# Kernel optimization log

Measured on AMD Instinct MI355X. Metric: run time of the kernel, lower is better.

## Reference

```python
import jax, jax.numpy as jnp
import numpy as np

HID = 4096
BLOCK = 64


def _masks(n=HID, bs=BLOCK):
    blk = jnp.arange(n) // bs
    mask_diag = (blk[:, None] == blk[None, :]).astype(jnp.float32)  # block-diagonal ones
    triu = (jnp.arange(n)[:, None] <= jnp.arange(n)[None, :]).astype(jnp.float32)
    mask_triu = triu * (1.0 - mask_diag)  # strictly above-block upper triangle
    return mask_diag, mask_triu


def _mc_linear(x, W, b, mask_diag, mask_triu):
    # A uses detached input (stop_gradient); B carries gradient through x.
    A = jax.lax.stop_gradient(x) @ (W * mask_triu)
    B = x @ (W * mask_diag)
    return A + B + b


def setup_inputs() -> dict:
    key = jax.random.key(0)
    ks = jax.random.split(key, 10)
    X = jax.random.normal(ks[0], (8192, 1024), dtype=jnp.float32)
    s_in = 1.0 / np.sqrt(1024)
    s_h = 1.0 / np.sqrt(HID)
    W0 = jax.random.normal(ks[1], (1024, HID), dtype=jnp.float32) * s_in
    b0 = jax.random.normal(ks[2], (HID,), dtype=jnp.float32) * s_in
    W1 = jax.random.normal(ks[3], (HID, HID), dtype=jnp.float32) * s_h
    b1 = jax.random.normal(ks[4], (HID,), dtype=jnp.float32) * s_h
    W2 = jax.random.normal(ks[5], (HID, HID), dtype=jnp.float32) * s_h
    b2 = jax.random.normal(ks[6], (HID,), dtype=jnp.float32) * s_h
    W3 = jax.random.normal(ks[7], (HID, HID), dtype=jnp.float32) * s_h
    b3 = jax.random.normal(ks[8], (HID,), dtype=jnp.float32) * s_h
    return {"X": X, "W0": W0, "b0": b0, "W1": W1, "b1": b1,
            "W2": W2, "b2": b2, "W3": W3, "b3": b3}


def reference(X, W0, b0, W1, b1, W2, b2, W3, b3):
    mask_diag, mask_triu = _masks()
    h = X @ W0 + b0  # [B, HID]
    for W, b in ((W1, b1), (W2, b2), (W3, b3)):
        h = jax.nn.relu(h)  # dropout=0.0 -> identity
        h = _mc_linear(h, W, b, mask_diag, mask_triu)
    y_pred = h[..., BLOCK - 1::BLOCK]  # [B, num_blocks]
    return y_pred[..., -1]  # level = -1 (default LEVEL)
```

## Files before the change

### kernel.cpp

```cpp
#include <hip/hip_runtime.h>

typedef unsigned short u16;
typedef __attribute__((ext_vector_type(8))) short short8;
typedef __attribute__((ext_vector_type(4))) float f32x4;
typedef __attribute__((ext_vector_type(4))) unsigned short us4;

__device__ __forceinline__ u16 f2bf(float f) {
    unsigned u = __float_as_uint(f);
    u += 0x7fffu + ((u >> 16) & 1u);
    return (u16)(u >> 16);
}
__device__ __forceinline__ float bf2f(u16 h) {
    return __uint_as_float(((unsigned)h) << 16);
}

__global__ __launch_bounds__(256) void k_cvt(const float* __restrict__ in,
                                             u16* __restrict__ out, long n) {
    long i = ((long)blockIdx.x * 256 + threadIdx.x) * 4;
    if (i >= n) return;
    float4 v = *(const float4*)(in + i);
    us4 o;
    o.x = f2bf(v.x); o.y = f2bf(v.y); o.z = f2bf(v.z); o.w = f2bf(v.w);
    *(us4*)(out + i) = o;
}

__global__ __launch_bounds__(256) void k_transpose(const float* __restrict__ W,
                                                   u16* __restrict__ Wt,
                                                   int K, int N, int mask) {
    __shared__ float tile[32][33];
    const int n0 = blockIdx.x * 32, k0 = blockIdx.y * 32;
    const int tx = threadIdx.x, ty = threadIdx.y;
    if (mask && ((k0 >> 6) > (n0 >> 6))) {
        if (k0 >= ((n0 >> 8) + 1) * 256) return;
#pragma unroll
        for (int j = 0; j < 32; j += 8)
            Wt[(size_t)(n0 + ty + j) * K + (k0 + tx)] = 0;
        return;
    }
#pragma unroll
    for (int j = 0; j < 32; j += 8)
        tile[ty + j][tx] = W[(size_t)(k0 + ty + j) * N + (n0 + tx)];
    __syncthreads();
#pragma unroll
    for (int j = 0; j < 32; j += 8)
        Wt[(size_t)(n0 + ty + j) * K + (k0 + tx)] = f2bf(tile[tx][ty + j]);
}

__global__ __launch_bounds__(256) void k_extract(const float* __restrict__ W3,
                                                 float* __restrict__ col, int N) {
    int k = blockIdx.x * 256 + threadIdx.x;
    col[k] = W3[(size_t)k * N + (N - 1)];
}

#define BM 256
#define BN 256
#define BK 32
#define BUFE 16384
#define GLDS(src, dst)                                                          \
    __builtin_amdgcn_global_load_lds(                                           \
        (const __attribute__((address_space(1))) void*)(src),                   \
        (__attribute__((address_space(3))) void*)(dst), 16, 0, 0)

__global__ __launch_bounds__(512, 2) void k_gemm(const u16* __restrict__ A,
                                                 const u16* __restrict__ Bt,
                                                 const float* __restrict__ bias,
                                                 u16* __restrict__ C,
                                                 int M, int N, int K, int varK) {
    __shared__ __align__(16) u16 lds[4 * BUFE];

    const int d = blockIdx.y * gridDim.x + blockIdx.x;
    int bx, by;
    if (varK) {
        bx = (int)gridDim.x - 1 - (d / (int)gridDim.y);
        by = d % (int)gridDim.y;
    } else {
        const int nwg = (int)(gridDim.x * gridDim.y);
        const int cpx = nwg >> 3;
        const int swz = (d & 7) * cpx + (d >> 3);
        bx = swz % (int)gridDim.x;
        by = swz / (int)gridDim.x;
    }

    const int tid = (int)threadIdx.x;
    const int lane = tid & 63, wv = tid >> 6;
    const int wm = wv >> 2, wn = wv & 3;
    const int keff = varK ? min(K, (bx + 1) * BN) : K;
    const int nt = keff >> 5;

    const u16* Ab = A + (size_t)by * BM * K;
    const u16* Bb = Bt + (size_t)bx * BN * K;

    const int tr = tid >> 2, ts = tid & 3;
    const int ss = ts ^ ((tr >> 1) & 3);
    const u16* aSrc = Ab + (size_t)tr * K + ss * 8;
    const u16* bSrc = Bb + (size_t)tr * K + ss * 8;

#define STA(tt, ci, dbuf) GLDS(aSrc + (size_t)(tt) * BK + (size_t)(ci) * 128 * K, \
                               lds + (dbuf) + (ci) * 4096 + tid * 8)
#define STB(tt, ci, dbuf) GLDS(bSrc + (size_t)(tt) * BK + (size_t)(ci) * 128 * K, \
                               lds + (dbuf) + 8192 + (ci) * 4096 + tid * 8)

    const int l15 = lane & 15;
    const int sw = (lane >> 4) ^ ((l15 >> 1) & 3);
    const int arow = wm * 128 + l15;
    const int brow = wn * 64 + l15;

#define RDA(dst, mfh, dbuf)                                                          \
    {                                                                                \
        _Pragma("unroll")                                                            \
        for (int i = 0; i < 4; ++i)                                                  \
            dst[i] = *(const short8*)(lds + (dbuf) + (arow + (mfh) * 64 + i * 16) * 32 \
                                      + sw * 8);                                     \
    }
#define RDB(dst, dbuf)                                                               \
    {                                                                                \
        _Pragma("unroll")                                                            \
        for (int nf = 0; nf < 4; ++nf)                                               \
            dst[nf] = *(const short8*)(lds + (dbuf) + 8192 + (brow + nf * 16) * 32   \
                                       + sw * 8);                                    \
    }
#define MFMA16(afS, bfS, mb)                                                         \
    {                                                                                \
        __builtin_amdgcn_s_setprio(1);                                              \
        _Pragma("unroll")                                                            \
        for (int i = 0; i < 4; ++i)                                                  \
            _Pragma("unroll")                                                        \
            for (int nf = 0; nf < 4; ++nf)                                           \
                acc[(mb) + i][nf] = __builtin_amdgcn_mfma_f32_16x16x32_bf16(         \
                    afS[i], bfS[nf], acc[(mb) + i][nf], 0, 0, 0);                    \
        __builtin_amdgcn_s_setprio(0);                                              \
    }
#define PHASE_END                                                 \
    __builtin_amdgcn_sched_barrier(0);                            \
    __builtin_amdgcn_s_barrier();                                 \
    __builtin_amdgcn_sched_barrier(0);
#define VMW(n)                                                    \
    __builtin_amdgcn_sched_barrier(0);                            \
    asm volatile("s_waitcnt vmcnt(" #n ")");                      \
    __builtin_amdgcn_sched_barrier(0);

    f32x4 acc[8][4];
#pragma unroll
    for (int i = 0; i < 8; ++i)
#pragma unroll
        for (int j = 0; j < 4; ++j)
            acc[i][j] = (f32x4){0.f, 0.f, 0.f, 0.f};

    short8 afX[4], afY[4], bfP[4], bfQ[4];

    STA(0, 0, 0);     STA(0, 1, 0);     STB(0, 0, 0);     STB(0, 1, 0);
    STA(1, 0, BUFE);  STA(1, 1, BUFE);  STB(1, 0, BUFE);  STB(1, 1, BUFE);
    STA(2, 0, 2*BUFE);STA(2, 1, 2*BUFE);STB(2, 0, 2*BUFE);STB(2, 1, 2*BUFE);
    VMW(8)
    __builtin_amdgcn_s_barrier();
    __builtin_amdgcn_sched_barrier(0);
    RDA(afX, 0, 0);
    RDB(bfP, 0);

    for (int T = 0; T < nt; T += 2) {
        const int U = T + 1;
        const int bT = (T & 3) * BUFE;
        const int bU = ((T + 1) & 3) * BUFE;
        const int bV = ((T + 2) & 3) * BUFE;
        const int bZ1 = ((T + 3) & 3) * BUFE;
        const int bZ2 = ((T + 4) & 3) * BUFE;
        RDA(afY, 1, bT);
        if (T + 3 < nt) { STA(T + 3, 0, bZ1); STA(T + 3, 1, bZ1); }
        MFMA16(afX, bfP, 0);
        if (T + 3 < nt) { VMW(6) } else { VMW(0) }
        PHASE_END;
        RDA(afX, 0, bU);
        RDB(bfQ, bU);
        if (T + 3 < nt) { STB(T + 3, 0, bZ1); STB(T + 3, 1, bZ1); }
        MFMA16(afY, bfP, 4);
        PHASE_END;
        RDA(afY, 1, bU);
        if (U + 3 < nt) { STA(U + 3, 0, bZ2); STA(U + 3, 1, bZ2); }
        MFMA16(afX, bfQ, 0);
        if (U + 1 < nt) {
            if (U + 3 < nt) { VMW(6) } else if (U + 2 < nt) { VMW(4) } else { VMW(0) }
        }
        PHASE_END;
        if (U + 1 < nt) {
            RDA(afX, 0, bV);
            RDB(bfP, bV);
        }
        if (U + 3 < nt) { STB(U + 3, 0, bZ2); STB(U + 3, 1, bZ2); }
        MFMA16(afY, bfQ, 4);
        PHASE_END;
    }

    const int rbase = by * BM + wm * 128 + (lane >> 4) * 4;
    const int cbase = bx * BN + wn * 64 + l15;
#pragma unroll
    for (int nf = 0; nf < 4; ++nf) {
        const int gc = cbase + nf * 16;
        const float bv = bias[gc];
#pragma unroll
        for (int mf = 0; mf < 8; ++mf) {
#pragma unroll
            for (int r = 0; r < 4; ++r) {
                int gr = rbase + mf * 16 + r;
                float h = acc[mf][nf][r] + bv;
                h = fmaxf(h, 0.0f);
                C[(size_t)gr * N + gc] = f2bf(h);
            }
        }
    }
#undef STA
#undef STB
#undef RDA
#undef RDB
#undef MFMA16
#undef PHASE_END
#undef VMW
}

__global__ __launch_bounds__(256) void k_matvec(const u16* __restrict__ act,
                                                const float* __restrict__ col,
                                                const float* __restrict__ b3,
                                                float* __restrict__ out, int K) {
    const int m = blockIdx.x, t = (int)threadIdx.x;
    const u16* row = act + (size_t)m * K;
    float acc = 0.f;
#pragma unroll
    for (int j = 0; j < 2; ++j) {
        int base = t * 16 + j * 8;
        short8 v = *(const short8*)(row + base);
#pragma unroll
        for (int u = 0; u < 8; ++u)
            acc += bf2f((u16)v[u]) * col[base + u];
    }
#pragma unroll
    for (int off = 32; off > 0; off >>= 1)
        acc += __shfl_down(acc, off);
    __shared__ float red[4];
    if ((t & 63) == 0) red[t >> 6] = acc;
    __syncthreads();
    if (t == 0) out[m] = red[0] + red[1] + red[2] + red[3] + b3[K - 1];
}

extern "C" void kernel_launch(void* const* d_in, const int* in_sizes, int n_in,
                              void* d_out, int out_size, void* d_ws, size_t ws_size,
                              hipStream_t stream) {
    const float* X  = (const float*)d_in[0];
    const float* W0 = (const float*)d_in[1];
    const float* b0 = (const float*)d_in[2];
    const float* W1 = (const float*)d_in[3];
    const float* b1 = (const float*)d_in[4];
    const float* W2 = (const float*)d_in[5];
    const float* b2 = (const float*)d_in[6];
    const float* W3 = (const float*)d_in[7];
    const float* b3 = (const float*)d_in[8];
    float* out = (float*)d_out;

    const int M = 8192, K0 = 1024, H = 4096;

    char* ws = (char*)d_ws;
    u16* Wt    = (u16*)(ws);
    u16* actA  = (u16*)(ws + 33554432);
    u16* actB  = (u16*)(ws + 33554432 + 67108864);
    u16* Xb    = actB;
    float* col = (float*)(ws + 33554432 + 2 * 67108864);

    k_cvt<<<dim3((M * K0) / 1024), 256, 0, stream>>>(X, Xb, (long)M * K0);
    k_transpose<<<dim3(H / 32, K0 / 32), dim3(32, 8), 0, stream>>>(W0, Wt, K0, H, 0);
    k_gemm<<<dim3(H / BN, M / BM), 512, 0, stream>>>(Xb, Wt, b0, actA, M, H, K0, 0);
    k_transpose<<<dim3(H / 32, H / 32), dim3(32, 8), 0, stream>>>(W1, Wt, H, H, 1);
    k_gemm<<<dim3(H / BN, M / BM), 512, 0, stream>>>(actA, Wt, b1, actB, M, H, H, 1);
    k_transpose<<<dim3(H / 32, H / 32), dim3(32, 8), 0, stream>>>(W2, Wt, H, H, 1);
    k_gemm<<<dim3(H / BN, M / BM), 512, 0, stream>>>(actB, Wt, b2, actA, M, H, H, 1);
    k_extract<<<dim3(H / 256), 256, 0, stream>>>(W3, col, H);
    k_matvec<<<dim3(M), 256, 0, stream>>>(actA, col, b3, out, H);
}
```

Before: 406.2 us.

## Switch GEMM inner loop from 16x16x32 to 32x32x16 bf16 MFMA

Replaces the per-wave 128x64 tile's 16x16x32 MFMA tiling with 32x32x16 MFMAs (4x2 fragments of f32x16 accumulators), splitting each 32-wide K tile into two K-halves per phase. LDS fragment reads and the swizzle indexing change to match the 32-row operand layout, the main loop drops from two tiles to one tile per iteration, and the epilogue row mapping is rewritten for the 32x32 output layout. The aim is fewer MFMA issues and fewer LDS fragment loads per FLOP, at the cost of a changed barrier cadence and different LDS bank-conflict behaviour.

```diff
diff --git a/kernel.cpp b/kernel.cpp
--- a/kernel.cpp
+++ b/kernel.cpp
@@ -2,7 +2,7 @@
 
 typedef unsigned short u16;
 typedef __attribute__((ext_vector_type(8))) short short8;
-typedef __attribute__((ext_vector_type(4))) float f32x4;
+typedef __attribute__((ext_vector_type(16))) float f32x16;
 typedef __attribute__((ext_vector_type(4))) unsigned short us4;
 
 __device__ __forceinline__ u16 f2bf(float f) {
@@ -100,34 +100,35 @@
 #define STB(tt, ci, dbuf) GLDS(bSrc + (size_t)(tt) * BK + (size_t)(ci) * 128 * K, \
                                lds + (dbuf) + 8192 + (ci) * 4096 + tid * 8)
 
-    const int l15 = lane & 15;
-    const int sw = (lane >> 4) ^ ((l15 >> 1) & 3);
-    const int arow = wm * 128 + l15;
-    const int brow = wn * 64 + l15;
-
-#define RDA(dst, mfh, dbuf)                                                          \
+    const int l31 = lane & 31, l5 = lane >> 5;
+    const int sw2 = (l31 >> 1) & 3;
+    const int sbase = l5 ^ sw2;
+    const int arow = wm * 128 + l31;
+    const int brow = wn * 64 + l31;
+
+#define RDA(dst, ks, dbuf)                                                           \
     {                                                                                \
         _Pragma("unroll")                                                            \
-        for (int i = 0; i < 4; ++i)                                                  \
-            dst[i] = *(const short8*)(lds + (dbuf) + (arow + (mfh) * 64 + i * 16) * 32 \
-                                      + sw * 8);                                     \
-    }
-#define RDB(dst, dbuf)                                                               \
+        for (int mf = 0; mf < 4; ++mf)                                               \
+            dst[mf] = *(const short8*)(lds + (dbuf) + (arow + mf * 32) * 32          \
+                                       + ((sbase ^ ((ks) << 1))) * 8);               \
+    }
+#define RDB(dst, ks, dbuf)                                                           \
     {                                                                                \
         _Pragma("unroll")                                                            \
-        for (int nf = 0; nf < 4; ++nf)                                               \
-            dst[nf] = *(const short8*)(lds + (dbuf) + 8192 + (brow + nf * 16) * 32   \
-                                       + sw * 8);                                    \
-    }
-#define MFMA16(afS, bfS, mb)                                                         \
+        for (int nf = 0; nf < 2; ++nf)                                               \
+            dst[nf] = *(const short8*)(lds + (dbuf) + 8192 + (brow + nf * 32) * 32   \
+                                       + ((sbase ^ ((ks) << 1))) * 8);               \
+    }
+#define MFMA8(afS, bfS)                                                              \
     {                                                                                \
         __builtin_amdgcn_s_setprio(1);                                              \
         _Pragma("unroll")                                                            \
-        for (int i = 0; i < 4; ++i)                                                  \
+        for (int mf = 0; mf < 4; ++mf)                                               \
             _Pragma("unroll")                                                        \
-            for (int nf = 0; nf < 4; ++nf)                                           \
-                acc[(mb) + i][nf] = __builtin_amdgcn_mfma_f32_16x16x32_bf16(         \
-                    afS[i], bfS[nf], acc[(mb) + i][nf], 0, 0, 0);                    \
+            for (int nf = 0; nf < 2; ++nf)                                           \
+                acc[mf][nf] = __builtin_amdgcn_mfma_f32_32x32x16_bf16(               \
+                    afS[mf], bfS[nf], acc[mf][nf], 0, 0, 0);                         \
         __builtin_amdgcn_s_setprio(0);                                              \
     }
 #define PHASE_END                                                 \
@@ -139,14 +140,16 @@
     asm volatile("s_waitcnt vmcnt(" #n ")");                      \
     __builtin_amdgcn_sched_barrier(0);
 
-    f32x4 acc[8][4];
-#pragma unroll
-    for (int i = 0; i < 8; ++i)
-#pragma unroll
-        for (int j = 0; j < 4; ++j)
-            acc[i][j] = (f32x4){0.f, 0.f, 0.f, 0.f};
-
-    short8 afX[4], afY[4], bfP[4], bfQ[4];
+    f32x16 acc[4][2];
+#pragma unroll
+    for (int i = 0; i < 4; ++i)
+#pragma unroll
+        for (int j = 0; j < 2; ++j)
+#pragma unroll
+            for (int r = 0; r < 16; ++r)
+                acc[i][j][r] = 0.f;
+
+    short8 afX[4], afY[4], bfX[2], bfY[2];
 
     STA(0, 0, 0);     STA(0, 1, 0);     STB(0, 0, 0);     STB(0, 1, 0);
     STA(1, 0, BUFE);  STA(1, 1, BUFE);  STB(1, 0, BUFE);  STB(1, 1, BUFE);
@@ -155,53 +158,41 @@
     __builtin_amdgcn_s_barrier();
     __builtin_amdgcn_sched_barrier(0);
     RDA(afX, 0, 0);
-    RDB(bfP, 0);
-
-    for (int T = 0; T < nt; T += 2) {
-        const int U = T + 1;
+    RDB(bfX, 0, 0);
+
+    for (int T = 0; T < nt; ++T) {
         const int bT = (T & 3) * BUFE;
-        const int bU = ((T + 1) & 3) * BUFE;
-        const int bV = ((T + 2) & 3) * BUFE;
-        const int bZ1 = ((T + 3) & 3) * BUFE;
-        const int bZ2 = ((T + 4) & 3) * BUFE;
+        const int bY = ((T + 1) & 3) * BUFE;
+        const int bZ = ((T + 3) & 3) * BUFE;
         RDA(afY, 1, bT);
-        if (T + 3 < nt) { STA(T + 3, 0, bZ1); STA(T + 3, 1, bZ1); }
-        MFMA16(afX, bfP, 0);
-        if (T + 3 < nt) { VMW(6) } else { VMW(0) }
-        PHASE_END;
-        RDA(afX, 0, bU);
-        RDB(bfQ, bU);
-        if (T + 3 < nt) { STB(T + 3, 0, bZ1); STB(T + 3, 1, bZ1); }
-        MFMA16(afY, bfP, 4);
-        PHASE_END;
-        RDA(afY, 1, bU);
-        if (U + 3 < nt) { STA(U + 3, 0, bZ2); STA(U + 3, 1, bZ2); }
-        MFMA16(afX, bfQ, 0);
-        if (U + 1 < nt) {
-            if (U + 3 < nt) { VMW(6) } else if (U + 2 < nt) { VMW(4) } else { VMW(0) }
+        RDB(bfY, 1, bT);
+        if (T + 3 < nt) { STA(T + 3, 0, bZ); STA(T + 3, 1, bZ); }
+        MFMA8(afX, bfX);
+        if (T + 1 < nt) {
+            if (T + 3 < nt) { VMW(6) } else if (T + 2 < nt) { VMW(4) } else { VMW(0) }
         }
         PHASE_END;
-        if (U + 1 < nt) {
-            RDA(afX, 0, bV);
-            RDB(bfP, bV);
+        if (T + 1 < nt) {
+            RDA(afX, 0, bY);
+            RDB(bfX, 0, bY);
         }
-        if (U + 3 < nt) { STB(U + 3, 0, bZ2); STB(U + 3, 1, bZ2); }
-        MFMA16(afY, bfQ, 4);
+        if (T + 3 < nt) { STB(T + 3, 0, bZ); STB(T + 3, 1, bZ); }
+        MFMA8(afY, bfY);
         PHASE_END;
     }
 
-    const int rbase = by * BM + wm * 128 + (lane >> 4) * 4;
-    const int cbase = bx * BN + wn * 64 + l15;
-#pragma unroll
-    for (int nf = 0; nf < 4; ++nf) {
-        const int gc = cbase + nf * 16;
+    const int rbase = by * BM + wm * 128 + 4 * l5;
+    const int cbase = bx * BN + wn * 64 + l31;
+#pragma unroll
+    for (int nf = 0; nf < 2; ++nf) {
+        const int gc = cbase + nf * 32;
         const float bv = bias[gc];
 #pragma unroll
-        for (int mf = 0; mf < 8; ++mf) {
-#pragma unroll
-            for (int r = 0; r < 4; ++r) {
-                int gr = rbase + mf * 16 + r;
-                float h = acc[mf][nf][r] + bv;
+        for (int mf = 0; mf < 4; ++mf) {
+#pragma unroll
+            for (int reg = 0; reg < 16; ++reg) {
+                int gr = rbase + mf * 32 + (reg & 3) + 8 * (reg >> 2);
+                float h = acc[mf][nf][reg] + bv;
                 h = fmaxf(h, 0.0f);
                 C[(size_t)gr * N + gc] = f2bf(h);
             }
@@ -211,7 +202,7 @@
 #undef STB
 #undef RDA
 #undef RDB
-#undef MFMA16
+#undef MFMA8
 #undef PHASE_END
 #undef VMW
 }
```

Measured after the change: 406.5 us. Within noise of the previous version (+0.1%).
